# Kernel optimization log

Measured on AMD Instinct MI355X. Metric: run time of the kernel, lower is better.

The kernel has to match this reference:

```python
import jax, jax.numpy as jnp
import numpy as np
import math

EMBED = 256
HEADS = 8
HD = EMBED // HEADS  # 32
NB = 3               # n_behaviors
C = NB * NB + 1      # 10 behavior-pair classes
NUM_BUCKETS = 32
MAX_DIST = 40
EPS = 1e-12
B, L = 4, 512


def _rel_bucket(seq_len, num_buckets=NUM_BUCKETS, max_distance=MAX_DIST):
    """T5-style relative position buckets, matching RelativePositionBias._relative_position_bucket."""
    pos = jnp.arange(seq_len)
    relative_position = pos[None, :] - pos[:, None]  # k - q
    n = -relative_position
    nb = num_buckets // 2
    ret = (n < 0).astype(jnp.int32) * nb
    n = jnp.abs(n)
    max_exact = nb // 2
    is_small = n < max_exact
    nf = jnp.maximum(n, 1).astype(jnp.float32)  # clamp to avoid log(0); masked by is_small anyway
    val_large = max_exact + (jnp.log(nf / max_exact) / math.log(max_distance / max_exact) * (nb - max_exact)).astype(jnp.int32)
    val_large = jnp.minimum(val_large, nb - 1)
    return ret + jnp.where(is_small, n, val_large)


def setup_inputs() -> dict:
    key = jax.random.key(0)
    ks = jax.random.split(key, 12)
    s = 0.02
    return {
        "input_tensor": jax.random.normal(ks[0], (B, L, EMBED), jnp.float32),
        "attention_mask": jnp.zeros((B, 1, L, L), jnp.float32),
        "type_seq": jax.random.randint(ks[1], (B, L), 0, NB + 1),
        "Wq": jax.random.normal(ks[2], (NB + 1, EMBED, HEADS, HD), jnp.float32) * s,
        "Wk": jax.random.normal(ks[3], (NB + 1, EMBED, HEADS, HD), jnp.float32) * s,
        "Wv": jax.random.normal(ks[4], (NB + 1, EMBED, HEADS, HD), jnp.float32) * s,
        "W1": jax.random.normal(ks[5], (NB, HEADS, HD, HD), jnp.float32) * s,
        "alpha1": jax.random.normal(ks[6], (C, NB, HEADS), jnp.float32),
        "W2": jax.random.normal(ks[7], (NB, HEADS, HD, HD), jnp.float32) * s,
        "alpha2": jax.random.normal(ks[8], (C, NB, HEADS), jnp.float32),
        "rp_tables": jax.random.normal(ks[9], (C, NUM_BUCKETS, HEADS), jnp.float32) * s,
        "ln_gamma": jnp.ones((EMBED,), jnp.float32),
        "ln_beta": jnp.zeros((EMBED,), jnp.float32),
    }


def reference(input_tensor, attention_mask, type_seq, Wq, Wk, Wv, W1, alpha1, W2, alpha2, rp_tables, ln_gamma, ln_beta):
    bsz, seq_len, emb = input_tensor.shape
    ts = type_seq
    # behavior pair matrix: 0 if either side is padding, else (tq-1)*NB + tk in [1, NB^2]
    bm = ((ts[:, :, None] * ts[:, None, :]) != 0).astype(jnp.int32)
    bm = bm * ((ts[:, :, None] - 1) * NB + ts[:, None, :])  # [B,L,L]

    # --- relative position bias, gathered per behavior pair ---
    bucket = _rel_bucket(seq_len)                 # [L,L]
    vals = rp_tables[:, bucket, :]                # [C,L,L,H]
    qi = jnp.arange(seq_len)[None, :, None]
    ki = jnp.arange(seq_len)[None, None, :]
    bias = vals[bm, qi, ki]                       # [B,L,L,H] gathered along C per pair
    bias = jnp.transpose(bias, (0, 3, 1, 2))      # [B,H,L,L]

    # --- behavior-gated QKV ---
    oh = jax.nn.one_hot(ts, NB + 1, dtype=input_tensor.dtype)  # [B,L,NB+1]
    q = jnp.einsum('BLH,bHhd,BLb->BhLd', input_tensor, Wq, oh)
    k = jnp.einsum('BLH,bHhd,BLb->BhLd', input_tensor, Wk, oh)
    v = jnp.einsum('BLH,bHhd,BLb->BhLd', input_tensor, Wv, oh)

    # --- bilinear scores with per-pair mixing matrices ---
    W1_ = jnp.einsum('bhmn,Cbh->Chmn', W1, jax.nn.softmax(alpha1, axis=1))
    att_all = jnp.einsum('BhQm,Chmn,BhKn->BhQKC', q, W1_, k)  # [B,H,L,L,C]
    scores = jnp.take_along_axis(att_all, bm[:, None, :, :, None], axis=4)[..., 0]
    scores = scores * (1.0 / math.sqrt(HD)) + bias + attention_mask
    probs = jax.nn.softmax(scores, axis=-1)  # dropout=0.0 -> identity

    # --- behavior-mixed value aggregation ---
    W2_ = jnp.einsum('bhmn,Cbh->Chmn', W2, jax.nn.softmax(alpha2, axis=1))
    oh_bm = jax.nn.one_hot(bm, C, dtype=probs.dtype)          # [B,L,L,C]
    pC = probs[:, :, :, :, None] * oh_bm[:, None]             # [B,H,L,L,C]
    ctx = jnp.einsum('BhQKC,Chnm,BhKn->BhQm', pC, W2_, v)     # [B,H,L,d]

    ctx = jnp.transpose(ctx, (0, 2, 1, 3)).reshape(bsz, seq_len, emb)
    x = ctx + input_tensor  # out_dropout=0.0
    mu = jnp.mean(x, axis=-1, keepdims=True)
    var = jnp.mean(jnp.square(x - mu), axis=-1, keepdims=True)
    return (x - mu) / jnp.sqrt(var + EPS) * ln_gamma + ln_beta
```

## Files before the change

kernel.cpp:

```cpp
#include <hip/hip_runtime.h>
#include <math.h>

#define BB 4
#define LL 512
#define EMB 256
#define NH 8
#define HD 32
#define NB_ 3
#define CCN 10
#define NBKT 32
#define SCALE 0.17677669529663687f

typedef __bf16 bf16_t;
typedef __attribute__((ext_vector_type(8))) bf16_t bf16x8;
typedef __attribute__((ext_vector_type(4))) float f32x4;

__device__ __forceinline__ unsigned short f2b(float f) {
    unsigned int u = __float_as_uint(f);
    u += 0x7FFF + ((u >> 16) & 1);
    return (unsigned short)(u >> 16);
}
__device__ __forceinline__ float b2f(unsigned short s) {
    return __uint_as_float(((unsigned int)s) << 16);
}
__device__ __forceinline__ unsigned pack2(float a, float b) {
    return (unsigned)f2b(a) | ((unsigned)f2b(b) << 16);
}
__device__ __forceinline__ int bm_of(int tq, int tk) {
    return (tq * tk != 0) ? ((tq - 1) * 3 + tk) : 0;
}
__device__ __forceinline__ unsigned long long shfl_up64(unsigned long long v, int d) {
    unsigned lo = (unsigned)__shfl_up((int)(unsigned)v, d, 64);
    unsigned hi = (unsigned)__shfl_up((int)(v >> 32), d, 64);
    return (((unsigned long long)hi) << 32) | lo;
}

__device__ __forceinline__ void sort512(const int* __restrict__ tsb, int* spk,
                                        unsigned long long* wtll, int* msc, int tid) {
    int ty0 = tsb[2 * tid], ty1 = tsb[2 * tid + 1];
    unsigned long long pk = (1ULL << (16 * ty0)) + (1ULL << (16 * ty1));
    unsigned long long v = pk;
    int lane = tid & 63;
#pragma unroll
    for (int off = 1; off < 64; off <<= 1) {
        unsigned long long o = shfl_up64(v, off);
        if (lane >= off) v += o;
    }
    int w = tid >> 6;
    if (lane == 63) wtll[w] = v;
    __syncthreads();
    unsigned long long pre = 0, tot = 0;
#pragma unroll
    for (int i = 0; i < 4; i++) {
        unsigned long long xx = wtll[i];
        if (i < w) pre += xx;
        tot += xx;
    }
    v += pre;
    unsigned long long excl = v - pk;
    int c0 = (int)(tot & 0xFFFF), c1 = (int)((tot >> 16) & 0xFFFF);
    int c2 = (int)((tot >> 32) & 0xFFFF), c3 = (int)((tot >> 48) & 0xFFFF);
    int ub0 = 0, ub1 = c0, ub2 = c0 + c1, ub3 = c0 + c1 + c2;
    if (tid == 0) {
        int pc0 = (c0 + 31) & ~31, pc1 = (c1 + 31) & ~31, pc2 = (c2 + 31) & ~31, pc3 = (c3 + 31) & ~31;
        int pb1 = pc0, pb2 = pc0 + pc1, pb3 = pc0 + pc1 + pc2;
        msc[0] = 0;  msc[1] = pb1; msc[2] = pb2; msc[3] = pb3;
        msc[4] = ub0; msc[5] = ub1; msc[6] = ub2; msc[7] = ub3;
        msc[8] = c0; msc[9] = c1; msc[10] = c2; msc[11] = c3;
        msc[12] = (pb3 + pc3 + 63) & ~63;
    }
    int bases[4] = {ub0, ub1, ub2, ub3};
    int r0 = (int)((excl >> (16 * ty0)) & 0xFFFF);
    unsigned long long excl1 = excl + (1ULL << (16 * ty0));
    int r1 = (int)((excl1 >> (16 * ty1)) & 0xFFFF);
    spk[bases[ty0] + r0] = (ty0 << 16) | (2 * tid);
    spk[bases[ty1] + r1] = (ty1 << 16) | (2 * tid + 1);
    __syncthreads();
}

__device__ __forceinline__ void pad_lookup(const int* msc, int pos, int& real, int& upos, int& seg) {
    seg = (pos >= msc[1]) + (pos >= msc[2]) + (pos >= msc[3]);
    int r = pos - msc[seg];
    real = (r < msc[8 + seg]) ? 1 : 0;
    upos = msc[4 + seg] + r;
}

__global__ void k_pre(const float* __restrict__ A1, const float* __restrict__ W1,
                      const float* __restrict__ A2, const float* __restrict__ W2,
                      const float* __restrict__ Wq, const float* __restrict__ Wk, const float* __restrict__ Wv,
                      const float* __restrict__ am, const int* __restrict__ ts,
                      float* __restrict__ W1s, float* __restrict__ W2s,
                      unsigned short* __restrict__ W1Tb, unsigned short* __restrict__ W2Tb,
                      unsigned short* __restrict__ Wt, int* __restrict__ mflagArr,
                      int* __restrict__ spkg, int* __restrict__ mscg, int* __restrict__ kpadg,
                      short* __restrict__ tblg) {
    __shared__ float cmb[32 * 33];
    __shared__ unsigned short ls[64 * 264];
    __shared__ int reds[4];
    __shared__ int spk_s[LL];
    __shared__ unsigned long long wtll[4];
    __shared__ int msc_s[16];
    int g = blockIdx.x, tid = threadIdx.x;
    if (g < 160) {
        int idx = g;
        const float* alpha = (idx < 80) ? A1 : A2;
        const float* W     = (idx < 80) ? W1 : W2;
        float* Ws          = (idx < 80) ? W1s : W2s;
        unsigned short* WT = (idx < 80) ? W1Tb : W2Tb;
        idx %= 80;
        int cc = idx / NH, h = idx % NH;
        float a0 = alpha[cc * NB_ * NH + 0 * NH + h];
        float a1 = alpha[cc * NB_ * NH + 1 * NH + h];
        float a2 = alpha[cc * NB_ * NH + 2 * NH + h];
        float mx = fmaxf(a0, fmaxf(a1, a2));
        float e0 = __expf(a0 - mx), e1 = __expf(a1 - mx), e2 = __expf(a2 - mx);
        float inv = 1.0f / (e0 + e1 + e2);
        e0 *= inv; e1 *= inv; e2 *= inv;
        for (int i = tid; i < HD * HD; i += 256) {
            int m = i >> 5, n = i & 31;
            float acc = e0 * W[((0 * NH + h) * HD + m) * HD + n]
                      + e1 * W[((1 * NH + h) * HD + m) * HD + n]
                      + e2 * W[((2 * NH + h) * HD + m) * HD + n];
            cmb[m * 33 + n] = acc;
        }
        __syncthreads();
        for (int i = tid; i < HD * HD; i += 256) {
            int a = i >> 5, bq = i & 31;
            Ws[((cc * NH + h) * HD + a) * HD + bq] = cmb[a * 33 + bq];
            WT[((size_t)(cc * NH + h) * HD + a) * HD + bq] = f2b(cmb[bq * 33 + a]);
        }
        return;
    }
    if (g < 208) {
        int t = g - 160;
        int tw = t >> 2, ob = t & 3;
        int which = tw >> 2, ty = tw & 3;
        const float* src = ((which == 0) ? Wq : (which == 1) ? Wk : Wv) + (size_t)ty * EMB * EMB;
        int out0 = ob * 64;
        for (int it = 0; it < 16; it++) {
            int e = it * 16 + (tid >> 4);
            int o4 = (tid & 15) * 4;
            float4 v = *(const float4*)&src[(size_t)e * EMB + out0 + o4];
            ls[(o4 + 0) * 264 + e] = f2b(v.x);
            ls[(o4 + 1) * 264 + e] = f2b(v.y);
            ls[(o4 + 2) * 264 + e] = f2b(v.z);
            ls[(o4 + 3) * 264 + e] = f2b(v.w);
        }
        __syncthreads();
        int out = tid >> 2, ech = (tid & 3) * 8;
        unsigned short* dst = Wt + (size_t)tw * EMB * EMB + (size_t)(out0 + out) * EMB;
        const unsigned short* srcl = &ls[out * 264];
#pragma unroll
        for (int jj = 0; jj < 8; jj++)
            *(uint4*)&dst[ech + jj * 32] = *(const uint4*)&srcl[ech + jj * 32];
        return;
    }
    if (g < 464) {
        int idx = g - 208;
        const uint4* p = (const uint4*)am + (size_t)idx * 1024;
        unsigned o = 0;
#pragma unroll
        for (int j = 0; j < 4; j++) {
            uint4 v = p[tid + j * 256];
            o |= v.x | v.y | v.z | v.w;
        }
        int wv = __any(o != 0);
        if ((tid & 63) == 0) reds[tid >> 6] = wv;
        __syncthreads();
        if (tid == 0) mflagArr[idx] = reds[0] | reds[1] | reds[2] | reds[3];
        return;
    }
    if (g < 468) {
        int b = g - 464;
        sort512(ts + b * LL, spk_s, wtll, msc_s, tid);
        for (int i = tid; i < LL; i += 256) spkg[b * LL + i] = spk_s[i];
        if (tid < 16) mscg[b * 16 + tid] = msc_s[tid];
        int KT = msc_s[12];
        for (int pos = tid; pos < KT; pos += 256) {
            int real, upos, seg;
            pad_lookup(msc_s, pos, real, upos, seg);
            int orig = real ? (spk_s[upos] & 0xFFFF) : 0x3FF;
            kpadg[b * 640 + pos] = (seg << 20) | ((real ? upos : 0) << 10) | orig;
        }
        return;
    }
    for (int d = tid; d < LL; d += 256) {
        int v;
        if (d < 8) v = d;
        else {
            double r = log((double)d / 8.0) / log(5.0);
            v = 8 + (int)(r * 8.0);
            if (v > 15) v = 15;
        }
        tblg[d] = (short)v;
    }
}

__global__ __launch_bounds__(256, 4) void k_qkv(
    const float* __restrict__ x, const int* __restrict__ spkg, const int* __restrict__ mscg,
    const unsigned short* __restrict__ Wt,
    unsigned short* __restrict__ qp, unsigned short* __restrict__ kp,
    unsigned short* __restrict__ vpT) {
    __shared__ int spk[LL];
    __shared__ int msc[16];
    __shared__ unsigned short vt_l[128 * 33];

    int g = blockIdx.x, tid = threadIdx.x;
    int ns = g % 6, gb = g / 6;
    int b = gb >> 4, tb = gb & 15, i0 = tb * 32;
    int which = ns >> 1, nh = ns & 1;
    int wave = tid >> 6, lane = tid & 63, quad = lane >> 4, col = lane & 15;

    spk[tid] = spkg[b * LL + tid];
    spk[tid + 256] = spkg[b * LL + tid + 256];
    if (tid < 16) msc[tid] = mscg[b * 16 + tid];
    __syncthreads();

    bf16x8 afr[2][8];
#pragma unroll
    for (int mt = 0; mt < 2; mt++) {
        int orig = spk[i0 + mt * 16 + col] & 0xFFFF;
        const float* xr = &x[(size_t)(b * LL + orig) * EMB];
#pragma unroll
        for (int kc = 0; kc < 8; kc++) {
            float4 v0 = *(const float4*)&xr[kc * 32 + quad * 8];
            float4 v1 = *(const float4*)&xr[kc * 32 + quad * 8 + 4];
            uint4 up;
            up.x = pack2(v0.x, v0.y); up.y = pack2(v0.z, v0.w);
            up.z = pack2(v1.x, v1.y); up.w = pack2(v1.z, v1.w);
            afr[mt][kc] = *(bf16x8*)&up;
        }
    }
    int t_start = spk[i0] >> 16, t_end = spk[i0 + 31] >> 16;
    unsigned short* outp = (which == 0) ? qp : kp;

    for (int ty = t_start; ty <= t_end; ty++) {
        f32x4 acc[2][2];
#pragma unroll
        for (int mt = 0; mt < 2; mt++)
#pragma unroll
            for (int nt = 0; nt < 2; nt++) acc[mt][nt] = (f32x4){0.f, 0.f, 0.f, 0.f};
        const unsigned short* wsrc = Wt + (size_t)(which * 4 + ty) * EMB * EMB + (size_t)(nh * 128) * EMB;
        const unsigned short* w0 = &wsrc[(size_t)((wave * 2 + 0) * 16 + col) * EMB + quad * 8];
        const unsigned short* w1 = &wsrc[(size_t)((wave * 2 + 1) * 16 + col) * EMB + quad * 8];
#pragma unroll
        for (int kc = 0; kc < 8; kc++) {
            bf16x8 b0 = *(const bf16x8*)&w0[kc * 32];
            bf16x8 b1 = *(const bf16x8*)&w1[kc * 32];
            acc[0][0] = __builtin_amdgcn_mfma_f32_16x16x32_bf16(afr[0][kc], b0, acc[0][0], 0, 0, 0);
            acc[0][1] = __builtin_amdgcn_mfma_f32_16x16x32_bf16(afr[0][kc], b1, acc[0][1], 0, 0, 0);
            acc[1][0] = __builtin_amdgcn_mfma_f32_16x16x32_bf16(afr[1][kc], b0, acc[1][0], 0, 0, 0);
            acc[1][1] = __builtin_amdgcn_mfma_f32_16x16x32_bf16(afr[1][kc], b1, acc[1][1], 0, 0, 0);
        }
        if (which < 2) {
#pragma unroll
            for (int mt = 0; mt < 2; mt++)
#pragma unroll
                for (int r = 0; r < 4; r++) {
                    int tokloc = mt * 16 + quad * 4 + r;
                    int tty = spk[i0 + tokloc] >> 16;
                    if (tty != ty) continue;
#pragma unroll
                    for (int nt = 0; nt < 2; nt++) {
                        int n = nh * 128 + (wave * 2 + nt) * 16 + col;
                        int h = n >> 5, d = n & 31;
                        outp[((size_t)(b * NH + h) * LL + i0 + tokloc) * HD + d] = f2b(acc[mt][nt][r]);
                    }
                }
        } else {
#pragma unroll
            for (int mt = 0; mt < 2; mt++)
#pragma unroll
                for (int nt = 0; nt < 2; nt++) {
                    int ln = (wave * 2 + nt) * 16 + col;
#pragma unroll
                    for (int r = 0; r < 4; r++)
                        vt_l[ln * 33 + mt * 16 + quad * 4 + r] = f2b(acc[mt][nt][r]);
                }
            __syncthreads();
            int ub = msc[4 + ty], cnt = msc[8 + ty], pb = msc[ty];
            int lo = ub - i0; if (lo < 0) lo = 0;
            int hi = ub + cnt - i0; if (hi > 32) hi = 32;
            int run = hi - lo;
            int pbase = pb + i0 + lo - ub;
            int rowbase = b * 256 + nh * 128;
            int t32 = tid & 31;
            if (t32 < run) {
                for (int rr = tid >> 5; rr < 128; rr += 8)
                    vpT[(size_t)(rowbase + rr) * 640 + pbase + t32] = vt_l[rr * 33 + lo + t32];
            }
            __syncthreads();
        }
    }
}

#define SCP 648
#define OFF_UN   20736
#define OFF_QTB  29184
#define OFF_KPAD 33536
#define OFF_TBL  36096
#define OFF_RPL  37120
#define OFF_QOR  38400
#define OFF_QTY  38464
#define OFF_INV  38528
#define SM_TOTAL 38592
__global__ __launch_bounds__(256, 4) void k_attn(
    const unsigned short* __restrict__ qp, const unsigned short* __restrict__ kp,
    const unsigned short* __restrict__ vpT,
    const int* __restrict__ spkg, const int* __restrict__ mscg, const int* __restrict__ kpadg,
    const short* __restrict__ tblg,
    const float* __restrict__ rp, const float* __restrict__ am,
    const float* __restrict__ W1s, const float* __restrict__ W2s,
    const unsigned short* __restrict__ W1Tb, const unsigned short* __restrict__ W2Tb,
    const int* __restrict__ mflagArr, float* __restrict__ ctx) {
    __shared__ __align__(16) char smem[SM_TOTAL];
    __shared__ int msk_s;
    unsigned short* scu = (unsigned short*)smem;
    unsigned short* qstb = (unsigned short*)(smem + OFF_UN);
    float* sb   = (float*)(smem + OFF_UN);
    unsigned short* qtb = (unsigned short*)(smem + OFF_QTB);
    unsigned short* sbb = (unsigned short*)(smem + OFF_QTB);
    int*   kpad = (int*)(smem + OFF_KPAD);
    short* tbl  = (short*)(smem + OFF_TBL);
    float* rp_l = (float*)(smem + OFF_RPL);
    int*   qor_l = (int*)(smem + OFF_QOR);
    int*   qty_l = (int*)(smem + OFF_QTY);
    float* inv_l = (float*)(smem + OFF_INV);

    int blk = blockIdx.x;
    int b = blk >> 8, h = (blk >> 5) & 7, q16 = blk & 31;
    int i0q = q16 * 16;
    int tid = threadIdx.x;
    int wave = tid >> 6, lane = tid & 63, quad = lane >> 4, col = lane & 15;
    int bh = b * NH + h;

    int KT = mscg[b * 16 + 12];
    if (wave == 0) {
        int v = 0;
#pragma unroll
        for (int j = 0; j < 4; j++) v |= mflagArr[lane + 64 * j];
        int anyv = __any(v != 0);
        if (lane == 0) msk_s = anyv;
    }
    if (tid < 16) {
        int v = spkg[b * LL + i0q + tid];
        qor_l[tid] = v & 0xFFFF; qty_l[tid] = v >> 16;
    }
    for (int pos = tid; pos < KT; pos += 256) kpad[pos] = kpadg[b * 640 + pos];
    ((int*)tbl)[tid] = ((const int*)tblg)[tid];
    for (int i = tid; i < CCN * NBKT; i += 256) rp_l[i] = rp[i * NH + h];
    {
        int q = tid >> 4, m2 = (tid & 15) * 2;
        ((unsigned*)qstb)[q * 20 + (tid & 15)] =
            *(const unsigned*)&qp[((size_t)bh * LL + i0q + q) * HD + m2];
    }
    __syncthreads();

    int qor_r[4], qty_r[4];
#pragma unroll
    for (int r = 0; r < 4; r++) { qor_r[r] = qor_l[quad * 4 + r]; qty_r[r] = qty_l[quad * 4 + r]; }
    bool uniq = (qty_l[0] == qty_l[15]);
    int tqu = qty_l[0];
    int mz = (msk_s == 0);

    if (uniq) {
#pragma unroll
        for (int it = 0; it < 2; it++) {
            int t8 = wave * 2 + it;
            int tk = t8 >> 1, nhf = t8 & 1;
            int bmv = bm_of(tqu, tk);
            bf16x8 a = *(const bf16x8*)&qstb[col * 40 + quad * 8];
            bf16x8 bb = *(const bf16x8*)&W1Tb[((size_t)(bmv * NH + h) * HD + nhf * 16 + col) * HD + quad * 8];
            f32x4 d = {0.f, 0.f, 0.f, 0.f};
            d = __builtin_amdgcn_mfma_f32_16x16x32_bf16(a, bb, d, 0, 0, 0);
#pragma unroll
            for (int r = 0; r < 4; r++)
                qtb[(quad * 4 + r) * 136 + tk * 32 + nhf * 16 + col] = f2b(d[r]);
        }
    } else {
        for (int i = tid; i < 16 * 128; i += 256) {
            int q = i >> 7, r = i & 127, tk = r >> 5, n = r & 31;
            int bmv = bm_of(qty_l[q], tk);
            const float* wb = &W1s[((bmv * NH + h) * HD) * HD + n];
            float acc = 0.f;
#pragma unroll
            for (int m = 0; m < HD; m++) acc += b2f(qstb[q * 40 + m]) * wb[m * HD];
            qtb[q * 136 + tk * 32 + n] = f2b(acc);
        }
    }
    __syncthreads();

    const float* amb = am + (size_t)b * LL * LL;
    int ntiles = KT >> 4;
    for (int tile = wave; tile < ntiles; tile += 4) {
        int kb = tile * 16;
        int kv0 = kpad[kb];
        if ((kv0 & 0x3FF) == 0x3FF) {
#pragma unroll
            for (int r = 0; r < 4; r++) scu[(quad * 4 + r) * SCP + kb + col] = 0xFF80;
            continue;
        }
        int tkt = kv0 >> 20;
        int kpi = kb + col;
        int kv = kpad[kpi];
        int ko = kv & 0x3FF;
        int upos = (kv >> 10) & 0x3FF;
        bool real = (ko != 0x3FF);
        bf16x8 bfr;
        if (real) bfr = *(const bf16x8*)&kp[((size_t)bh * LL + upos) * HD + quad * 8];
        else { uint4 z = make_uint4(0, 0, 0, 0); bfr = *(bf16x8*)&z; }
        bf16x8 a = *(const bf16x8*)&qtb[col * 136 + tkt * 32 + quad * 8];
        f32x4 d = {0.f, 0.f, 0.f, 0.f};
        d = __builtin_amdgcn_mfma_f32_16x16x32_bf16(a, bfr, d, 0, 0, 0);
        if (!real) {
#pragma unroll
            for (int r = 0; r < 4; r++) scu[(quad * 4 + r) * SCP + kpi] = 0xFF80;
        } else {
#pragma unroll
            for (int r = 0; r < 4; r++) {
                int q = quad * 4 + r;
                int qo = qor_r[r];
                int dd = qo - ko;
                int ad = dd < 0 ? -dd : dd;
                int bk = (dd < 0 ? 16 : 0) + (int)tbl[ad];
                float sv = d[r] * SCALE + rp_l[bm_of(qty_r[r], tkt) * NBKT + bk];
                if (!mz) sv += amb[(size_t)qo * LL + ko];
                scu[q * SCP + kpi] = f2b(sv);
            }
        }
    }
    __syncthreads();

    {
        int gq = tid >> 4, t16 = tid & 15;
        float mx = -1e30f;
        for (int kk = t16; kk < KT; kk += 16) mx = fmaxf(mx, b2f(scu[gq * SCP + kk]));
#pragma unroll
        for (int off = 1; off < 16; off <<= 1) mx = fmaxf(mx, __shfl_xor(mx, off, 16));
        float sum = 0.f;
        for (int kk = t16; kk < KT; kk += 16) {
            int idx = gq * SCP + kk;
            float e = __expf(b2f(scu[idx]) - mx);
            scu[idx] = f2b(e); sum += e;
        }
#pragma unroll
        for (int off = 1; off < 16; off <<= 1) sum += __shfl_xor(sum, off, 16);
        if (t16 == 0) inv_l[gq] = 1.0f / sum;
    }
    __syncthreads();

    f32x4 accv[4][2];
#pragma unroll
    for (int t = 0; t < 4; t++)
#pragma unroll
        for (int hh = 0; hh < 2; hh++) accv[t][hh] = (f32x4){0.f, 0.f, 0.f, 0.f};

    const unsigned short* vbase = &vpT[(size_t)(b * 256 + h * 32) * 640];
    int ngroups = KT >> 5;
    for (int gg = wave; gg < ngroups; gg += 4) {
        int loc = gg << 5;
        int kvg = kpad[loc];
        if ((kvg & 0x3FF) == 0x3FF) continue;
        int tk = kvg >> 20;
        bf16x8 a = *(const bf16x8*)&scu[col * SCP + loc + quad * 8];
        bf16x8 b0 = *(const bf16x8*)&vbase[(size_t)col * 640 + loc + quad * 8];
        bf16x8 b1 = *(const bf16x8*)&vbase[(size_t)(col + 16) * 640 + loc + quad * 8];
        if (tk == 0) {
            accv[0][0] = __builtin_amdgcn_mfma_f32_16x16x32_bf16(a, b0, accv[0][0], 0, 0, 0);
            accv[0][1] = __builtin_amdgcn_mfma_f32_16x16x32_bf16(a, b1, accv[0][1], 0, 0, 0);
        } else if (tk == 1) {
            accv[1][0] = __builtin_amdgcn_mfma_f32_16x16x32_bf16(a, b0, accv[1][0], 0, 0, 0);
            accv[1][1] = __builtin_amdgcn_mfma_f32_16x16x32_bf16(a, b1, accv[1][1], 0, 0, 0);
        } else if (tk == 2) {
            accv[2][0] = __builtin_amdgcn_mfma_f32_16x16x32_bf16(a, b0, accv[2][0], 0, 0, 0);
            accv[2][1] = __builtin_amdgcn_mfma_f32_16x16x32_bf16(a, b1, accv[2][1], 0, 0, 0);
        } else {
            accv[3][0] = __builtin_amdgcn_mfma_f32_16x16x32_bf16(a, b0, accv[3][0], 0, 0, 0);
            accv[3][1] = __builtin_amdgcn_mfma_f32_16x16x32_bf16(a, b1, accv[3][1], 0, 0, 0);
        }
    }
    __syncthreads();

#pragma unroll
    for (int w = 0; w < 4; w++) {
        if (wave == w) {
#pragma unroll
            for (int t = 0; t < 4; t++)
#pragma unroll
                for (int hh = 0; hh < 2; hh++)
#pragma unroll
                    for (int r = 0; r < 4; r++) {
                        int q = quad * 4 + r;
                        int n = col + 16 * hh;
                        float val = accv[t][hh][r];
                        if (w == 0) {
                            sb[q * 132 + t * 32 + n] = val;
                        } else if (w < 3) {
                            sb[q * 132 + t * 32 + n] += val;
                        } else {
                            float fin = sb[q * 132 + t * 32 + n] + val;
                            sb[q * 132 + t * 32 + n] = fin;
                            sbb[q * 136 + t * 32 + n] = f2b(fin);
                        }
                    }
        }
        __syncthreads();
    }

    if (uniq) {
        if (wave < 2) {
            int mhf = wave;
            f32x4 d = {0.f, 0.f, 0.f, 0.f};
#pragma unroll
            for (int tk = 0; tk < 4; tk++) {
                int bmv = bm_of(tqu, tk);
                bf16x8 a = *(const bf16x8*)&sbb[col * 136 + tk * 32 + quad * 8];
                bf16x8 bb = *(const bf16x8*)&W2Tb[((size_t)(bmv * NH + h) * HD + mhf * 16 + col) * HD + quad * 8];
                d = __builtin_amdgcn_mfma_f32_16x16x32_bf16(a, bb, d, 0, 0, 0);
            }
#pragma unroll
            for (int r = 0; r < 4; r++) {
                int q = quad * 4 + r;
                ctx[((size_t)(b * LL + qor_l[q])) * EMB + h * HD + mhf * 16 + col] = d[r] * inv_l[q];
            }
        }
    } else {
        int m = tid & 31, qq = tid >> 5;
#pragma unroll
        for (int rep = 0; rep < 2; rep++) {
            int qi = qq + 8 * rep;
            int tq = qty_l[qi];
            float acc = 0.f;
#pragma unroll
            for (int tk2 = 0; tk2 < 4; tk2++) {
                int bmv = bm_of(tq, tk2);
                const float* wb = &W2s[((bmv * NH + h) * HD) * HD + m];
                const float* sbp = &sb[qi * 132 + tk2 * 32];
                for (int n = 0; n < HD; n++) acc += sbp[n] * wb[n * HD];
            }
            int qo = qor_l[qi];
            ctx[((size_t)(b * LL + qo)) * EMB + h * HD + m] = acc * inv_l[qi];
        }
    }
}

__global__ void k_ln(const float* __restrict__ ctx, const float* __restrict__ x,
                     const float* __restrict__ gamma, const float* __restrict__ beta,
                     float* __restrict__ out) {
    __shared__ float red[8];
    __shared__ float red2[8];
    int blk = blockIdx.x;
    int b = blk >> 9, l = blk & 511;
    int j = threadIdx.x;
    size_t base = ((size_t)(b * LL + l)) * EMB;
    float v = ctx[base + j] + x[base + j];
    float s = v, s2 = v * v;
    for (int off = 32; off > 0; off >>= 1) { s += __shfl_down(s, off, 64); s2 += __shfl_down(s2, off, 64); }
    int wid = j >> 6;
    if ((j & 63) == 0) { red[wid] = s; red2[wid] = s2; }
    __syncthreads();
    if (j == 0) {
        float ts_ = 0, ts2 = 0;
        for (int w = 0; w < 4; w++) { ts_ += red[w]; ts2 += red2[w]; }
        red[4] = ts_; red2[4] = ts2;
    }
    __syncthreads();
    float mu = red[4] / (float)EMB;
    float var = red2[4] / (float)EMB - mu * mu;
    float r = rsqrtf(var + 1e-12f);
    out[base + j] = (v - mu) * r * gamma[j] + beta[j];
}

extern "C" void kernel_launch(void* const* d_in, const int* in_sizes, int n_in,
                              void* d_out, int out_size, void* d_ws, size_t ws_size,
                              hipStream_t stream) {
    const float* x  = (const float*)d_in[0];
    const float* am = (const float*)d_in[1];
    const int*   ts = (const int*)d_in[2];
    const float* Wq = (const float*)d_in[3];
    const float* Wk = (const float*)d_in[4];
    const float* Wv = (const float*)d_in[5];
    const float* W1 = (const float*)d_in[6];
    const float* a1 = (const float*)d_in[7];
    const float* W2 = (const float*)d_in[8];
    const float* a2 = (const float*)d_in[9];
    const float* rp = (const float*)d_in[10];
    const float* g  = (const float*)d_in[11];
    const float* be = (const float*)d_in[12];
    float* out = (float*)d_out;

    float* ws  = (float*)d_ws;
    float* W1s = ws;
    float* W2s = ws + 81920;
    unsigned short* W1Tb = (unsigned short*)(ws + 163840);
    unsigned short* W2Tb = (unsigned short*)(ws + 204800);
    int* mflagArr = (int*)(ws + 245760);
    int* spkg = (int*)(ws + 246016);
    int* mscg = (int*)(ws + 248064);
    int* kpadg = (int*)(ws + 248128);
    short* tblg = (short*)(ws + 250688);
    unsigned short* qp = (unsigned short*)(ws + 250944);
    unsigned short* kp = qp + BB * NH * LL * HD;
    unsigned short* vpT = kp + BB * NH * LL * HD;
    float* ctx = (float*)(vpT + BB * 256 * 640);
    unsigned short* Wt = (unsigned short*)ctx;

    hipLaunchKernelGGL(k_pre, dim3(469), dim3(256), 0, stream,
                       a1, W1, a2, W2, Wq, Wk, Wv, am, ts, W1s, W2s, W1Tb, W2Tb, Wt,
                       mflagArr, spkg, mscg, kpadg, tblg);
    hipLaunchKernelGGL(k_qkv, dim3(384), dim3(256), 0, stream, x, spkg, mscg, Wt, qp, kp, vpT);
    hipLaunchKernelGGL(k_attn, dim3(BB * NH * 32), dim3(256), 0, stream,
                       qp, kp, vpT, spkg, mscg, kpadg, tblg, rp, am, W1s, W2s, W1Tb, W2Tb, mflagArr, ctx);
    hipLaunchKernelGGL(k_ln, dim3(BB * LL), dim3(256), 0, stream, ctx, x, g, be, out);
}
```

Baseline: 139.1 us.

## Add two-type MFMA fast path, per-type PV ranges, wave-per-token layernorm

Adds an MFMA path for query tiles holding exactly two behavior types, replacing the scalar fallback for those tiles in both the W1 projection and the W2 output. Reworks the PV accumulation so each wave handles one key-type segment using precomputed segment offsets from mscg, which removes per-group branching and the serialized four-wave reduction through shared memory. Rewrites layernorm to process one token per wave with float4 loads and shuffle-only reductions, with four tokens per block. Correctness depends on mscg holding segment start and count per key type, with wave index as the type.

```diff
diff --git a/kernel.cpp b/kernel.cpp
--- a/kernel.cpp
+++ b/kernel.cpp
@@ -361,6 +361,16 @@
     for (int r = 0; r < 4; r++) { qor_r[r] = qor_l[quad * 4 + r]; qty_r[r] = qty_l[quad * 4 + r]; }
     bool uniq = (qty_l[0] == qty_l[15]);
     int tqu = qty_l[0];
+    int tA = qty_l[0], tB = qty_l[15];
+    bool two = false;
+    if (!uniq) {
+        two = true;
+#pragma unroll
+        for (int i = 0; i < 16; i++) {
+            int t = qty_l[i];
+            two = two && (t == tA || t == tB);
+        }
+    }
     int mz = (msk_s == 0);
 
     if (uniq) {
@@ -376,6 +386,24 @@
 #pragma unroll
             for (int r = 0; r < 4; r++)
                 qtb[(quad * 4 + r) * 136 + tk * 32 + nhf * 16 + col] = f2b(d[r]);
+        }
+    } else if (two) {
+#pragma unroll
+        for (int it = 0; it < 2; it++) {
+            int t8 = wave * 2 + it;
+            int tk = t8 >> 1, nhf = t8 & 1;
+            bf16x8 a = *(const bf16x8*)&qstb[col * 40 + quad * 8];
+            bf16x8 bA = *(const bf16x8*)&W1Tb[((size_t)(bm_of(tA, tk) * NH + h) * HD + nhf * 16 + col) * HD + quad * 8];
+            bf16x8 bBv = *(const bf16x8*)&W1Tb[((size_t)(bm_of(tB, tk) * NH + h) * HD + nhf * 16 + col) * HD + quad * 8];
+            f32x4 dA = {0.f, 0.f, 0.f, 0.f};
+            f32x4 dB = {0.f, 0.f, 0.f, 0.f};
+            dA = __builtin_amdgcn_mfma_f32_16x16x32_bf16(a, bA, dA, 0, 0, 0);
+            dB = __builtin_amdgcn_mfma_f32_16x16x32_bf16(a, bBv, dB, 0, 0, 0);
+#pragma unroll
+            for (int r = 0; r < 4; r++) {
+                float val = (qty_r[r] == tA) ? dA[r] : dB[r];
+                qtb[(quad * 4 + r) * 136 + tk * 32 + nhf * 16 + col] = f2b(val);
+            }
         }
     } else {
         for (int i = tid; i < 16 * 128; i += 256) {
@@ -449,63 +477,33 @@
     }
     __syncthreads();
 
-    f32x4 accv[4][2];
-#pragma unroll
-    for (int t = 0; t < 4; t++)
-#pragma unroll
-        for (int hh = 0; hh < 2; hh++) accv[t][hh] = (f32x4){0.f, 0.f, 0.f, 0.f};
-
     const unsigned short* vbase = &vpT[(size_t)(b * 256 + h * 32) * 640];
-    int ngroups = KT >> 5;
-    for (int gg = wave; gg < ngroups; gg += 4) {
-        int loc = gg << 5;
-        int kvg = kpad[loc];
-        if ((kvg & 0x3FF) == 0x3FF) continue;
-        int tk = kvg >> 20;
-        bf16x8 a = *(const bf16x8*)&scu[col * SCP + loc + quad * 8];
-        bf16x8 b0 = *(const bf16x8*)&vbase[(size_t)col * 640 + loc + quad * 8];
-        bf16x8 b1 = *(const bf16x8*)&vbase[(size_t)(col + 16) * 640 + loc + quad * 8];
-        if (tk == 0) {
-            accv[0][0] = __builtin_amdgcn_mfma_f32_16x16x32_bf16(a, b0, accv[0][0], 0, 0, 0);
-            accv[0][1] = __builtin_amdgcn_mfma_f32_16x16x32_bf16(a, b1, accv[0][1], 0, 0, 0);
-        } else if (tk == 1) {
-            accv[1][0] = __builtin_amdgcn_mfma_f32_16x16x32_bf16(a, b0, accv[1][0], 0, 0, 0);
-            accv[1][1] = __builtin_amdgcn_mfma_f32_16x16x32_bf16(a, b1, accv[1][1], 0, 0, 0);
-        } else if (tk == 2) {
-            accv[2][0] = __builtin_amdgcn_mfma_f32_16x16x32_bf16(a, b0, accv[2][0], 0, 0, 0);
-            accv[2][1] = __builtin_amdgcn_mfma_f32_16x16x32_bf16(a, b1, accv[2][1], 0, 0, 0);
-        } else {
-            accv[3][0] = __builtin_amdgcn_mfma_f32_16x16x32_bf16(a, b0, accv[3][0], 0, 0, 0);
-            accv[3][1] = __builtin_amdgcn_mfma_f32_16x16x32_bf16(a, b1, accv[3][1], 0, 0, 0);
-        }
-    }
-    __syncthreads();
-
-#pragma unroll
-    for (int w = 0; w < 4; w++) {
-        if (wave == w) {
-#pragma unroll
-            for (int t = 0; t < 4; t++)
-#pragma unroll
-                for (int hh = 0; hh < 2; hh++)
-#pragma unroll
-                    for (int r = 0; r < 4; r++) {
-                        int q = quad * 4 + r;
-                        int n = col + 16 * hh;
-                        float val = accv[t][hh][r];
-                        if (w == 0) {
-                            sb[q * 132 + t * 32 + n] = val;
-                        } else if (w < 3) {
-                            sb[q * 132 + t * 32 + n] += val;
-                        } else {
-                            float fin = sb[q * 132 + t * 32 + n] + val;
-                            sb[q * 132 + t * 32 + n] = fin;
-                            sbb[q * 136 + t * 32 + n] = f2b(fin);
-                        }
-                    }
-        }
-        __syncthreads();
-    }
+    f32x4 accv[2];
+    accv[0] = (f32x4){0.f, 0.f, 0.f, 0.f};
+    accv[1] = (f32x4){0.f, 0.f, 0.f, 0.f};
+    {
+        int pb = mscg[b * 16 + wave];
+        int cnt = mscg[b * 16 + 8 + wave];
+        int g0 = pb >> 5, g1 = (pb + cnt + 31) >> 5;
+        for (int gg = g0; gg < g1; ++gg) {
+            int loc = gg << 5;
+            bf16x8 a = *(const bf16x8*)&scu[col * SCP + loc + quad * 8];
+            bf16x8 b0 = *(const bf16x8*)&vbase[(size_t)col * 640 + loc + quad * 8];
+            bf16x8 b1 = *(const bf16x8*)&vbase[(size_t)(col + 16) * 640 + loc + quad * 8];
+            accv[0] = __builtin_amdgcn_mfma_f32_16x16x32_bf16(a, b0, accv[0], 0, 0, 0);
+            accv[1] = __builtin_amdgcn_mfma_f32_16x16x32_bf16(a, b1, accv[1], 0, 0, 0);
+        }
+    }
+#pragma unroll
+    for (int hh = 0; hh < 2; hh++)
+#pragma unroll
+        for (int r = 0; r < 4; r++) {
+            int q = quad * 4 + r, n = col + 16 * hh;
+            float fin = accv[hh][r];
+            sb[q * 132 + wave * 32 + n] = fin;
+            sbb[q * 136 + wave * 32 + n] = f2b(fin);
+        }
+    __syncthreads();
 
     if (uniq) {
         if (wave < 2) {
@@ -523,6 +521,23 @@
                 int q = quad * 4 + r;
                 ctx[((size_t)(b * LL + qor_l[q])) * EMB + h * HD + mhf * 16 + col] = d[r] * inv_l[q];
             }
+        }
+    } else if (two) {
+        int myT = (wave < 2) ? tA : tB;
+        int mhf = wave & 1;
+        f32x4 d = {0.f, 0.f, 0.f, 0.f};
+#pragma unroll
+        for (int tk = 0; tk < 4; tk++) {
+            int bmv = bm_of(myT, tk);
+            bf16x8 a = *(const bf16x8*)&sbb[col * 136 + tk * 32 + quad * 8];
+            bf16x8 bb = *(const bf16x8*)&W2Tb[((size_t)(bmv * NH + h) * HD + mhf * 16 + col) * HD + quad * 8];
+            d = __builtin_amdgcn_mfma_f32_16x16x32_bf16(a, bb, d, 0, 0, 0);
+        }
+#pragma unroll
+        for (int r = 0; r < 4; r++) {
+            int q = quad * 4 + r;
+            if (qty_l[q] == myT)
+                ctx[((size_t)(b * LL + qor_l[q])) * EMB + h * HD + mhf * 16 + col] = d[r] * inv_l[q];
         }
     } else {
         int m = tid & 31, qq = tid >> 5;
@@ -547,28 +562,31 @@
 __global__ void k_ln(const float* __restrict__ ctx, const float* __restrict__ x,
                      const float* __restrict__ gamma, const float* __restrict__ beta,
                      float* __restrict__ out) {
-    __shared__ float red[8];
-    __shared__ float red2[8];
-    int blk = blockIdx.x;
-    int b = blk >> 9, l = blk & 511;
-    int j = threadIdx.x;
-    size_t base = ((size_t)(b * LL + l)) * EMB;
-    float v = ctx[base + j] + x[base + j];
-    float s = v, s2 = v * v;
-    for (int off = 32; off > 0; off >>= 1) { s += __shfl_down(s, off, 64); s2 += __shfl_down(s2, off, 64); }
-    int wid = j >> 6;
-    if ((j & 63) == 0) { red[wid] = s; red2[wid] = s2; }
-    __syncthreads();
-    if (j == 0) {
-        float ts_ = 0, ts2 = 0;
-        for (int w = 0; w < 4; w++) { ts_ += red[w]; ts2 += red2[w]; }
-        red[4] = ts_; red2[4] = ts2;
-    }
-    __syncthreads();
-    float mu = red[4] / (float)EMB;
-    float var = red2[4] / (float)EMB - mu * mu;
+    int wave = threadIdx.x >> 6, lane = threadIdx.x & 63;
+    int tok = blockIdx.x * 4 + wave;
+    size_t base = (size_t)tok * EMB + lane * 4;
+    float4 c = *(const float4*)&ctx[base];
+    float4 xi = *(const float4*)&x[base];
+    float4 v;
+    v.x = c.x + xi.x; v.y = c.y + xi.y; v.z = c.z + xi.z; v.w = c.w + xi.w;
+    float s = v.x + v.y + v.z + v.w;
+    float s2 = v.x * v.x + v.y * v.y + v.z * v.z + v.w * v.w;
+#pragma unroll
+    for (int off = 1; off < 64; off <<= 1) {
+        s += __shfl_xor(s, off, 64);
+        s2 += __shfl_xor(s2, off, 64);
+    }
+    float mu = s * (1.0f / EMB);
+    float var = s2 * (1.0f / EMB) - mu * mu;
     float r = rsqrtf(var + 1e-12f);
-    out[base + j] = (v - mu) * r * gamma[j] + beta[j];
+    float4 gg = *(const float4*)&gamma[lane * 4];
+    float4 bb = *(const float4*)&beta[lane * 4];
+    float4 o;
+    o.x = (v.x - mu) * r * gg.x + bb.x;
+    o.y = (v.y - mu) * r * gg.y + bb.y;
+    o.z = (v.z - mu) * r * gg.z + bb.z;
+    o.w = (v.w - mu) * r * gg.w + bb.w;
+    *(float4*)&out[base] = o;
 }
 
 extern "C" void kernel_launch(void* const* d_in, const int* in_sizes, int n_in,
@@ -611,5 +629,5 @@
     hipLaunchKernelGGL(k_qkv, dim3(384), dim3(256), 0, stream, x, spkg, mscg, Wt, qp, kp, vpT);
     hipLaunchKernelGGL(k_attn, dim3(BB * NH * 32), dim3(256), 0, stream,
                        qp, kp, vpT, spkg, mscg, kpadg, tblg, rp, am, W1s, W2s, W1Tb, W2Tb, mflagArr, ctx);
-    hipLaunchKernelGGL(k_ln, dim3(BB * LL), dim3(256), 0, stream, ctx, x, g, be, out);
-}
+    hipLaunchKernelGGL(k_ln, dim3(BB * LL / 4), dim3(256), 0, stream, ctx, x, g, be, out);
+}
```

After: 127.5 us. 1.09x faster.
